# Kernel optimization log

Measured on AMD Instinct MI355X. Metric: run time of the kernel, lower is better.

Reference implementation:

```python
import jax, jax.numpy as jnp
import numpy as np

NEG_SLOPE = 0.2

def gat_conv(x, src, dst, W, a_src, a_dst, bias, num_nodes, heads, out_ch, concat):
    # x: [N, Fin]; W: [Fin, heads*out_ch]; a_src/a_dst: [heads, out_ch]
    h = (x @ W).reshape(num_nodes, heads, out_ch)            # [N,H,C]
    alpha_s = jnp.einsum('nhc,hc->nh', h, a_src)             # [N,H]
    alpha_d = jnp.einsum('nhc,hc->nh', h, a_dst)             # [N,H]
    e = alpha_s[src] + alpha_d[dst]                          # [E,H]
    e = jnp.where(e > 0, e, NEG_SLOPE * e)                   # LeakyReLU
    # segment softmax over incoming edges per destination node
    m = jax.ops.segment_max(e, dst, num_segments=num_nodes)  # [N,H]
    m = jnp.where(jnp.isfinite(m), m, 0.0)
    ee = jnp.exp(e - m[dst])                                 # [E,H]
    s = jax.ops.segment_sum(ee, dst, num_segments=num_nodes) # [N,H]
    alpha = ee / (s[dst] + 1e-16)                            # [E,H]
    out = jax.ops.segment_sum(h[src] * alpha[:, :, None], dst,
                              num_segments=num_nodes)        # [N,H,C]
    if concat:
        out = out.reshape(num_nodes, heads * out_ch)
    else:
        out = out.mean(axis=1)
    return out + bias


def setup_inputs() -> dict:
    key = jax.random.key(0)
    ks = jax.random.split(key, 10)
    N, E = 50000, 800000
    EMB, HID, HEADS, REPR = 128, 128, 8, 64
    C1 = HID // HEADS  # 16
    x = jax.random.normal(ks[0], (N, EMB), dtype=jnp.float32)
    edge_index = jax.random.randint(ks[1], (2, E), 0, N, dtype=jnp.int32)
    sc = 1.0 / np.sqrt(EMB)
    W1 = jax.random.normal(ks[2], (EMB, HEADS * C1), dtype=jnp.float32) * sc
    a1_src = jax.random.normal(ks[3], (HEADS, C1), dtype=jnp.float32) * 0.1
    a1_dst = jax.random.normal(ks[4], (HEADS, C1), dtype=jnp.float32) * 0.1
    b1 = jnp.zeros((HID,), dtype=jnp.float32)
    sc2 = 1.0 / np.sqrt(HID)
    W2 = jax.random.normal(ks[5], (HID, REPR), dtype=jnp.float32) * sc2
    a2_src = jax.random.normal(ks[6], (1, REPR), dtype=jnp.float32) * 0.1
    a2_dst = jax.random.normal(ks[7], (1, REPR), dtype=jnp.float32) * 0.1
    b2 = jnp.zeros((REPR,), dtype=jnp.float32)
    return {"x": x, "edge_index": edge_index,
            "W1": W1, "a1_src": a1_src, "a1_dst": a1_dst, "b1": b1,
            "W2": W2, "a2_src": a2_src, "a2_dst": a2_dst, "b2": b2}


def reference(x, edge_index, W1, a1_src, a1_dst, b1, W2, a2_src, a2_dst, b2):
    N = x.shape[0]
    # PyG GATConv adds self-loops by default
    loops = jnp.arange(N, dtype=edge_index.dtype)
    src = jnp.concatenate([edge_index[0], loops])
    dst = jnp.concatenate([edge_index[1], loops])
    # eval mode: F.dropout(p=0.6) is identity
    h = gat_conv(x, src, dst, W1, a1_src, a1_dst, b1, N,
                 heads=8, out_ch=16, concat=True)
    h = jax.nn.elu(h)
    out = gat_conv(h, src, dst, W2, a2_src, a2_dst, b2, N,
                   heads=1, out_ch=64, concat=True)
    return out
```

## Files before the change

kernel.cpp:

```cpp
#include <hip/hip_runtime.h>
#include <hip/hip_fp16.h>
#include <math.h>


typedef _Float16 f16x8 __attribute__((ext_vector_type(8)));
typedef float f32x4 __attribute__((ext_vector_type(4)));

#define NCHUNK 8
#define MAXBDIV 8192
#define CAP 16384

__device__ __forceinline__ float leaky_exp(float e) {
    e = (e > 0.f) ? e : 0.2f * e;
    return __expf(e);
}

__device__ __forceinline__ void acc16(float w, float4 hv0, float4 hv1,
                                      float* __restrict__ acc) {
    const __half2* p0 = (const __half2*)&hv0;
    const __half2* p1 = (const __half2*)&hv1;
#pragma unroll
    for (int k = 0; k < 4; k++) {
        float2 f = __half22float2(p0[k]);
        acc[2 * k] += w * f.x;
        acc[2 * k + 1] += w * f.y;
    }
#pragma unroll
    for (int k = 0; k < 4; k++) {
        float2 f = __half22float2(p1[k]);
        acc[8 + 2 * k] += w * f.x;
        acc[8 + 2 * k + 1] += w * f.y;
    }
}

__device__ __forceinline__ void acc8(float w, float4 hv,
                                     float* __restrict__ acc) {
    const __half2* hp = (const __half2*)&hv;
#pragma unroll
    for (int k = 0; k < 4; k++) {
        float2 f = __half22float2(hp[k]);
        acc[2 * k] += w * f.x;
        acc[2 * k + 1] += w * f.y;
    }
}

__global__ __launch_bounds__(256) void augw_kernel(const float* __restrict__ W1,
                                                   const float* __restrict__ a1s,
                                                   const float* __restrict__ a1d,
                                                   const float* __restrict__ W2,
                                                   const float* __restrict__ a2s,
                                                   const float* __restrict__ a2d,
                                                   _Float16* __restrict__ W1t,
                                                   _Float16* __restrict__ W2t) {
    int t = threadIdx.x;
    if (blockIdx.x == 0) {
        for (int i = t; i < 144 * 128; i += 256) {
            int c = i >> 7, k = i & 127;
            float v;
            if (c < 128) {
                v = W1[k * 128 + c];
            } else if (c < 136) {
                int h = c - 128; v = 0.f;
#pragma unroll
                for (int j = 0; j < 16; j++) v += W1[k * 128 + h * 16 + j] * a1s[h * 16 + j];
            } else {
                int h = c - 136; v = 0.f;
#pragma unroll
                for (int j = 0; j < 16; j++) v += W1[k * 128 + h * 16 + j] * a1d[h * 16 + j];
            }
            W1t[c * 128 + k] = (_Float16)v;
        }
    } else {
        for (int i = t; i < 80 * 128; i += 256) {
            int c = i >> 7, k = i & 127;
            float v = 0.f;
            if (c < 64) {
                v = W2[k * 64 + c];
            } else if (c == 64) {
                for (int j = 0; j < 64; j++) v += W2[k * 64 + j] * a2s[j];
            } else if (c == 65) {
                for (int j = 0; j < 64; j++) v += W2[k * 64 + j] * a2d[j];
            }
            W2t[c * 128 + k] = (_Float16)v;
        }
    }
}

__global__ __launch_bounds__(256) void gemm1_bucket_kernel(
        const float* __restrict__ x, const _Float16* __restrict__ W1t,
        __half* __restrict__ h1, float* __restrict__ als,
        float* __restrict__ ald, int N, int gridG1,
        const int* __restrict__ src, const int* __restrict__ dst, int E,
        int* __restrict__ bucketCnt, unsigned* __restrict__ pairs) {
    __shared__ _Float16 Xs[64 * 136];
    int t = threadIdx.x;
    if ((int)blockIdx.x >= gridG1) {
        int* lcnt = (int*)Xs;
        int* lbase = lcnt + 64;
        if (t < 64) lcnt[t] = 0;
        __syncthreads();
        int bid = blockIdx.x - gridG1;
        int bdiv = (N + 7) >> 3;
        int i0 = (bid * 256 + t) * 4;
        int s_[4], d_[4], bk[4], rk[4];
        int nv = 0;
        if (i0 + 3 < E) {
            int4 d4 = *(const int4*)(dst + i0);
            int4 s4 = *(const int4*)(src + i0);
            s_[0] = s4.x; s_[1] = s4.y; s_[2] = s4.z; s_[3] = s4.w;
            d_[0] = d4.x; d_[1] = d4.y; d_[2] = d4.z; d_[3] = d4.w;
            nv = 4;
        } else {
            for (int k = i0; k < E && nv < 4; k++) {
                s_[nv] = src[k]; d_[nv] = dst[k]; nv++;
            }
        }
#pragma unroll 4
        for (int u = 0; u < 4; u++) {
            if (u < nv) {
                int b = (s_[u] / bdiv) * 8 + (d_[u] / bdiv);
                bk[u] = b;
                rk[u] = atomicAdd(&lcnt[b], 1);
            }
        }
        __syncthreads();
        if (t < 64) lbase[t] = atomicAdd(&bucketCnt[t * 16], lcnt[t]);
        __syncthreads();
#pragma unroll 4
        for (int k = 0; k < nv; k++) {
            unsigned dlocal = (unsigned)(d_[k] % bdiv);
            pairs[(size_t)bk[k] * CAP + lbase[bk[k]] + rk[k]] =
                (dlocal << 16) | (unsigned)s_[k];
        }
        return;
    }
    int row0 = blockIdx.x * 64;
    for (int i = t; i < 2048; i += 256) {
        int r = i >> 5, c4 = i & 31;
        int gr = row0 + r;
        float4 v = make_float4(0.f, 0.f, 0.f, 0.f);
        if (gr < N) v = *(const float4*)(x + (size_t)gr * 128 + c4 * 4);
        _Float16* dp = Xs + r * 136 + c4 * 4;
        dp[0] = (_Float16)v.x; dp[1] = (_Float16)v.y;
        dp[2] = (_Float16)v.z; dp[3] = (_Float16)v.w;
    }
    __syncthreads();
    int w = t >> 6, L = t & 63, m = L & 15, quad = L >> 4;
    f32x4 acc[9];
#pragma unroll
    for (int f = 0; f < 9; f++) acc[f] = (f32x4){0.f, 0.f, 0.f, 0.f};
    const _Float16* Arow = Xs + (w * 16 + m) * 136 + quad * 8;
    const _Float16* Brow = W1t + m * 128 + quad * 8;
#pragma unroll
    for (int kt = 0; kt < 4; kt++) {
        f16x8 a = *(const f16x8*)(Arow + kt * 32);
#pragma unroll
        for (int f = 0; f < 9; f++) {
            f16x8 b = *(const f16x8*)(Brow + f * 2048 + kt * 32);
            acc[f] = __builtin_amdgcn_mfma_f32_16x16x32_f16(a, b, acc[f], 0, 0, 0);
        }
    }
    int nbase = row0 + w * 16 + quad * 4;
#pragma unroll
    for (int r = 0; r < 4; r++) {
        int n = nbase + r;
        if (n < N) {
            __half* hrow = h1 + (size_t)n * 128 + m;
#pragma unroll
            for (int f = 0; f < 8; f++) hrow[f * 16] = __float2half(acc[f][r]);
            float v = acc[8][r];
            if (m < 8) als[n * 8 + m] = v;
            else ald[n * 8 + (m - 8)] = v;
        }
    }
}

__global__ __launch_bounds__(256) void subhist_kernel(
        const int* __restrict__ bucketCnt, const unsigned* __restrict__ pairs,
        int N, int* __restrict__ subcnt) {
    __shared__ int hist[MAXBDIV];
    int t = threadIdx.x;
    int b = blockIdx.x & 63;
    int j = blockIdx.x >> 6;
    int bdiv = (N + 7) >> 3;
    for (int i = t; i < bdiv; i += 256) hist[i] = 0;
    __syncthreads();
    int cnt = bucketCnt[b * 16];
    int chunk = (cnt + NCHUNK - 1) / NCHUNK;
    int lo = j * chunk;
    int hi = min(lo + chunk, cnt);
    const unsigned* plist = pairs + (size_t)b * CAP;
    for (int i = lo + t; i < hi; i += 256) {
        atomicAdd(&hist[plist[i] >> 16], 1);
    }
    __syncthreads();
    int* out = subcnt + (size_t)(b * NCHUNK + j) * bdiv;
    for (int i = t; i < bdiv; i += 256) out[i] = hist[i];
}

__global__ __launch_bounds__(256) void scan1_kernel(const int* __restrict__ subcnt,
                                                    int N,
                                                    int* __restrict__ rowstart,
                                                    int* __restrict__ blocksum) {
    __shared__ int tmp[256];
    int t = threadIdx.x;
    int i = blockIdx.x * 256 + t;
    int bdiv = (N + 7) >> 3;
    int v = 0;
    if (i < N) {
        int dd = i / bdiv;
        int local = i - dd * bdiv;
#pragma unroll
        for (int so = 0; so < 8; so++) {
            const int* sc = subcnt + ((size_t)(so * 8 + dd) * NCHUNK) * bdiv + local;
#pragma unroll
            for (int j = 0; j < NCHUNK; j++) v += sc[(size_t)j * bdiv];
        }
    }
    tmp[t] = v;
    __syncthreads();
    for (int off = 1; off < 256; off <<= 1) {
        int x = (t >= off) ? tmp[t - off] : 0;
        __syncthreads();
        tmp[t] += x;
        __syncthreads();
    }
    if (i < N) rowstart[i] = tmp[t] - v;
    if (t == 255) blocksum[blockIdx.x] = tmp[t];
}

__global__ __launch_bounds__(256) void scan23_kernel(int* __restrict__ rowstart,
                                                     const int* __restrict__ blocksum,
                                                     int nb,
                                                     int* __restrict__ subcnt,
                                                     int N, int E) {
    __shared__ int sdata[256];
    int t = threadIdx.x;
    int bx = blockIdx.x;
    sdata[t] = (t < nb && t < bx) ? blocksum[t] : 0;
    __syncthreads();
#pragma unroll
    for (int off = 128; off > 0; off >>= 1) {
        if (t < off) sdata[t] += sdata[t + off];
        __syncthreads();
    }
    int offset = sdata[0];
    int i = bx * 256 + t;
    int bdiv = (N + 7) >> 3;
    if (i < N) {
        int v = rowstart[i] + offset;
        rowstart[i] = v;
        int dd = i / bdiv;
        int local = i - dd * bdiv;
        int c = v;
#pragma unroll
        for (int so = 0; so < 8; so++) {
            int* sc = subcnt + ((size_t)(so * 8 + dd) * NCHUNK) * bdiv + local;
#pragma unroll
            for (int j = 0; j < NCHUNK; j++) {
                int cj = sc[(size_t)j * bdiv];
                sc[(size_t)j * bdiv] = c;
                c += cj;
            }
        }
    } else if (i == N) {
        rowstart[N] = E;
    }
}

__global__ __launch_bounds__(256) void scatter_kernel(
        const int* __restrict__ bucketCnt, const unsigned* __restrict__ pairs,
        int N, const int* __restrict__ subcnt, int* __restrict__ esrc) {
    __shared__ int lcur[MAXBDIV];
    int t = threadIdx.x;
    int b = blockIdx.x & 63;
    int j = blockIdx.x >> 6;
    int bdiv = (N + 7) >> 3;
    const int* base = subcnt + (size_t)(b * NCHUNK + j) * bdiv;
    for (int i = t; i < bdiv; i += 256) lcur[i] = base[i];
    __syncthreads();
    int cnt = bucketCnt[b * 16];
    int chunk = (cnt + NCHUNK - 1) / NCHUNK;
    int lo = j * chunk;
    int hi = min(lo + chunk, cnt);
    const unsigned* plist = pairs + (size_t)b * CAP;
    for (int i = lo + t; i < hi; i += 256) {
        unsigned p = plist[i];
        int pos = atomicAdd(&lcur[p >> 16], 1);
        esrc[pos] = (int)(p & 0xFFFFu);
    }
}

__global__ __launch_bounds__(256) void agg1_gemm2_kernel(
        const __half* __restrict__ h1, const float* __restrict__ als,
        const float* __restrict__ ald, const int* __restrict__ rowstart,
        const int* __restrict__ esrc, const float* __restrict__ b1,
        const _Float16* __restrict__ W2t, __half* __restrict__ h2,
        float* __restrict__ al2s, float* __restrict__ al2d, int N) {
    __shared__ _Float16 actS[32 * 136];
    int t = threadIdx.x;
    int lane = t & 63;
    int grp = lane >> 3;
    int q = lane & 7;
    int bdiv = (N + 7) >> 3;
    int lrow = (t >> 6) * 8 + grp;
    int ln = (blockIdx.x >> 3) * 32 + lrow;
    int n = (blockIdx.x & 7) * bdiv + ln;
    bool valid = (ln < bdiv) && (n < N);
    const float4* h1v = (const float4*)h1;
    float acc[16];
#pragma unroll
    for (int k = 0; k < 16; k++) acc[k] = 0.f;
    float wsum = 0.f;
    int beg = 0, end = 0;
    float adv = 0.f;
    if (valid) {
        adv = ald[n * 8 + q];
        float wself = leaky_exp(als[n * 8 + q] + adv);
        wsum = wself;
        acc16(wself, h1v[(size_t)n * 16 + 2 * q], h1v[(size_t)n * 16 + 2 * q + 1], acc);
        beg = rowstart[n];
        end = rowstart[n + 1];
    }
    int j = beg;
    for (; j + 4 <= end; j += 4) {
        int s0 = esrc[j], s1 = esrc[j + 1], s2 = esrc[j + 2], s3 = esrc[j + 3];
        float4 a0 = h1v[(size_t)s0 * 16 + 2 * q], b0 = h1v[(size_t)s0 * 16 + 2 * q + 1];
        float4 a1 = h1v[(size_t)s1 * 16 + 2 * q], b1v = h1v[(size_t)s1 * 16 + 2 * q + 1];
        float4 a2 = h1v[(size_t)s2 * 16 + 2 * q], b2 = h1v[(size_t)s2 * 16 + 2 * q + 1];
        float4 a3 = h1v[(size_t)s3 * 16 + 2 * q], b3 = h1v[(size_t)s3 * 16 + 2 * q + 1];
        float e0 = als[s0 * 8 + q], e1 = als[s1 * 8 + q];
        float e2 = als[s2 * 8 + q], e3 = als[s3 * 8 + q];
        float w0 = leaky_exp(e0 + adv), w1 = leaky_exp(e1 + adv);
        float w2 = leaky_exp(e2 + adv), w3 = leaky_exp(e3 + adv);
        wsum += (w0 + w1) + (w2 + w3);
        acc16(w0, a0, b0, acc);
        acc16(w1, a1, b1v, acc);
        acc16(w2, a2, b2, acc);
        acc16(w3, a3, b3, acc);
    }
    for (; j < end; j++) {
        int s = esrc[j];
        float w = leaky_exp(als[s * 8 + q] + adv);
        wsum += w;
        acc16(w, h1v[(size_t)s * 16 + 2 * q], h1v[(size_t)s * 16 + 2 * q + 1], acc);
    }
    __align__(16) __half2 po[8];
    if (valid) {
        float inv = 1.f / (wsum + 1e-16f);
        const float* bf = b1 + q * 16;
#pragma unroll
        for (int k = 0; k < 8; k++) {
            float o0 = acc[2 * k] * inv + bf[2 * k];
            float o1 = acc[2 * k + 1] * inv + bf[2 * k + 1];
            o0 = (o0 > 0.f) ? o0 : (__expf(o0) - 1.f);
            o1 = (o1 > 0.f) ? o1 : (__expf(o1) - 1.f);
            po[k] = __floats2half2_rn(o0, o1);
        }
    } else {
#pragma unroll
        for (int k = 0; k < 8; k++) po[k] = __floats2half2_rn(0.f, 0.f);
    }
    *(float4*)(actS + lrow * 136 + q * 16) = ((float4*)po)[0];
    *(float4*)(actS + lrow * 136 + q * 16 + 8) = ((float4*)po)[1];
    __syncthreads();
    int w4 = t >> 6;
    int m = lane & 15, quad = lane >> 4;
    int rt = w4 & 1;
    int ctbase = (w4 < 2) ? 0 : 1;
    f32x4 acc2[3];
#pragma unroll
    for (int f = 0; f < 3; f++) acc2[f] = (f32x4){0.f, 0.f, 0.f, 0.f};
    const _Float16* Arow2 = actS + (rt * 16 + m) * 136 + quad * 8;
    const _Float16* Brow2 = W2t + m * 128 + quad * 8;
#pragma unroll
    for (int kt = 0; kt < 4; kt++) {
        f16x8 a = *(const f16x8*)(Arow2 + kt * 32);
#pragma unroll
        for (int f = 0; f < 3; f++) {
            int ctf = ctbase + 2 * f;
            if (ctf < 5) {
                f16x8 bb = *(const f16x8*)(Brow2 + ctf * 2048 + kt * 32);
                acc2[f] = __builtin_amdgcn_mfma_f32_16x16x32_f16(a, bb, acc2[f], 0, 0, 0);
            }
        }
    }
    int secbase = (blockIdx.x & 7) * bdiv;
    int lnbase = (blockIdx.x >> 3) * 32 + rt * 16 + quad * 4;
#pragma unroll
    for (int r = 0; r < 4; r++) {
        int ln2 = lnbase + r;
        int n2 = secbase + ln2;
        if (ln2 < bdiv && n2 < N) {
#pragma unroll
            for (int f = 0; f < 3; f++) {
                int ctf = ctbase + 2 * f;
                if (ctf < 4) {
                    h2[(size_t)n2 * 64 + ctf * 16 + m] = __float2half(acc2[f][r]);
                } else if (ctf == 4) {
                    if (m == 0) al2s[n2] = acc2[f][r];
                    else if (m == 1) al2d[n2] = acc2[f][r];
                }
            }
        }
    }
}

__global__ __launch_bounds__(256) void agg2_kernel(const __half* __restrict__ h2,
                                                   const float* __restrict__ al2s,
                                                   const float* __restrict__ al2d,
                                                   const int* __restrict__ rowstart,
                                                   const int* __restrict__ esrc,
                                                   const float* __restrict__ b2,
                                                   float* __restrict__ out, int N) {
    int t = threadIdx.x;
    int lane = t & 63;
    int grp = lane >> 3;
    int q = lane & 7;
    int bdiv = (N + 7) >> 3;
    int ln = (blockIdx.x >> 3) * 32 + (t >> 6) * 8 + grp;
    if (ln >= bdiv) return;
    int n = (blockIdx.x & 7) * bdiv + ln;
    if (n >= N) return;
    const float4* h2v = (const float4*)h2;
    float adv = al2d[n];
    float acc[8];
#pragma unroll
    for (int k = 0; k < 8; k++) acc[k] = 0.f;
    float wsum = 0.f;
    {
        float w = leaky_exp(al2s[n] + adv);
        wsum += w;
        acc8(w, h2v[(size_t)n * 8 + q], acc);
    }
    int beg = rowstart[n], end = rowstart[n + 1];
    int j = beg;
    for (; j + 4 <= end; j += 4) {
        int s0 = esrc[j], s1 = esrc[j + 1], s2 = esrc[j + 2], s3 = esrc[j + 3];
        float4 a0 = h2v[(size_t)s0 * 8 + q];
        float4 a1 = h2v[(size_t)s1 * 8 + q];
        float4 a2 = h2v[(size_t)s2 * 8 + q];
        float4 a3 = h2v[(size_t)s3 * 8 + q];
        float e0 = al2s[s0], e1 = al2s[s1], e2 = al2s[s2], e3 = al2s[s3];
        float w0 = leaky_exp(e0 + adv), w1 = leaky_exp(e1 + adv);
        float w2 = leaky_exp(e2 + adv), w3 = leaky_exp(e3 + adv);
        wsum += (w0 + w1) + (w2 + w3);
        acc8(w0, a0, acc);
        acc8(w1, a1, acc);
        acc8(w2, a2, acc);
        acc8(w3, a3, acc);
    }
    for (; j < end; j++) {
        int s = esrc[j];
        float w = leaky_exp(al2s[s] + adv);
        wsum += w;
        acc8(w, h2v[(size_t)s * 8 + q], acc);
    }
    float inv = 1.f / (wsum + 1e-16f);
    const float* bf = b2 + q * 8;
    float4* ov = (float4*)(out + (size_t)n * 64 + q * 8);
    ov[0] = make_float4(acc[0] * inv + bf[0], acc[1] * inv + bf[1],
                        acc[2] * inv + bf[2], acc[3] * inv + bf[3]);
    ov[1] = make_float4(acc[4] * inv + bf[4], acc[5] * inv + bf[5],
                        acc[6] * inv + bf[6], acc[7] * inv + bf[7]);
}

extern "C" void kernel_launch(void* const* d_in, const int* in_sizes, int n_in,
                              void* d_out, int out_size, void* d_ws, size_t ws_size,
                              hipStream_t stream) {
    (void)n_in; (void)out_size; (void)ws_size;
    const float* x   = (const float*)d_in[0];
    const int*   ei  = (const int*)d_in[1];
    const float* W1  = (const float*)d_in[2];
    const float* a1s = (const float*)d_in[3];
    const float* a1d = (const float*)d_in[4];
    const float* b1  = (const float*)d_in[5];
    const float* W2  = (const float*)d_in[6];
    const float* a2s = (const float*)d_in[7];
    const float* a2d = (const float*)d_in[8];
    const float* b2  = (const float*)d_in[9];
    float* out = (float*)d_out;

    const int N = in_sizes[0] / 128;
    const int E = in_sizes[1] / 2;
    const int* src = ei;
    const int* dst = ei + E;
    const int bdiv = (N + 7) / 8;

    char* wp = (char*)d_ws;
    auto alloc = [&](size_t bytes) -> void* {
        void* p = (void*)wp;
        wp += (bytes + 255) & ~(size_t)255;
        return p;
    };
    __half* h1   = (__half*)alloc((size_t)N * 128 * 2);
    __half* h2   = (__half*)alloc((size_t)N * 64 * 2 + 64 * 256);
    float* al1s = (float*)alloc((size_t)N * 8 * 4);
    float* al1d = (float*)alloc((size_t)N * 8 * 4);
    float* al2s = (float*)alloc((size_t)N * 4);
    float* al2d = (float*)alloc((size_t)N * 4);
    int* bucketCnt = (int*)alloc(64 * 16 * 4);
    int* subcnt   = (int*)alloc((size_t)64 * NCHUNK * bdiv * 4);
    int* rowstart = (int*)alloc((size_t)(N + 1) * 4);
    int* esrc     = (int*)alloc((size_t)E * 4);
    unsigned* pairs = (unsigned*)alloc((size_t)64 * CAP * 4);
    int* blocksum = (int*)alloc(256 * 4);
    _Float16* W1t = (_Float16*)alloc(144 * 128 * 2);
    _Float16* W2t = (_Float16*)alloc(80 * 128 * 2);

    const int nbScan = (N + 255) / 256;
    const int gridH  = (E + 1023) / 1024;
    const int gridG1 = (N + 63) / 64;
    const int gridAggN = 8 * ((bdiv + 31) / 32);
    const int gridSort = 64 * NCHUNK;

    hipMemsetAsync(bucketCnt, 0, 64 * 16 * 4, stream);

    augw_kernel<<<2, 256, 0, stream>>>(W1, a1s, a1d, W2, a2s, a2d, W1t, W2t);
    gemm1_bucket_kernel<<<gridG1 + gridH, 256, 0, stream>>>(
        x, W1t, h1, al1s, al1d, N, gridG1, src, dst, E, bucketCnt, pairs);
    subhist_kernel<<<gridSort, 256, 0, stream>>>(bucketCnt, pairs, N, subcnt);
    scan1_kernel<<<nbScan, 256, 0, stream>>>(subcnt, N, rowstart, blocksum);
    scan23_kernel<<<(N + 256) / 256, 256, 0, stream>>>(rowstart, blocksum, nbScan,
                                                       subcnt, N, E);
    scatter_kernel<<<gridSort, 256, 0, stream>>>(bucketCnt, pairs, N, subcnt, esrc);

    agg1_gemm2_kernel<<<gridAggN, 256, 0, stream>>>(h1, al1s, al1d, rowstart, esrc,
                                                    b1, W2t, h2, al2s, al2d, N);
    agg2_kernel<<<gridAggN, 256, 0, stream>>>(h2, al2s, al2d, rowstart, esrc, b2, out, N);
}
```

Baseline: 222.7 us.

## Fuse CSR sort/scan/scatter kernels into one cooperative kernel with grid syncs

Replaces four separate launches (subhistogram, two scan passes, scatter) with a single cooperative kernel that uses grid.sync between phases, and halves NCHUNK so the grid is 256 blocks. This removes three kernel launch gaps and shortens the per-node subcount scan loops. The trade-offs are fewer blocks per phase, which means less parallelism in the atomic histogram and scatter, plus the cost of the grid-wide barriers. The cooperative launch also needs all 256 blocks to be co-resident despite the 32KB of LDS each block uses.

After: 339.3 us. 1.52x slower.

```diff
diff --git a/kernel.cpp b/kernel.cpp
--- a/kernel.cpp
+++ b/kernel.cpp
@@ -1,12 +1,15 @@
 #include <hip/hip_runtime.h>
 #include <hip/hip_fp16.h>
+#include <hip/hip_cooperative_groups.h>
 #include <math.h>
+
+namespace cg = cooperative_groups;
 
 
 typedef _Float16 f16x8 __attribute__((ext_vector_type(8)));
 typedef float f32x4 __attribute__((ext_vector_type(4)));
 
-#define NCHUNK 8
+#define NCHUNK 4
 #define MAXBDIV 8192
 #define CAP 16384
 
@@ -175,119 +178,103 @@
     }
 }
 
-__global__ __launch_bounds__(256) void subhist_kernel(
+__global__ __launch_bounds__(256) void sort_kernel(
         const int* __restrict__ bucketCnt, const unsigned* __restrict__ pairs,
-        int N, int* __restrict__ subcnt) {
-    __shared__ int hist[MAXBDIV];
+        int N, int E, int* __restrict__ subcnt, int* __restrict__ rowstart,
+        int* __restrict__ blocksum, int* __restrict__ esrc) {
+    cg::grid_group grid = cg::this_grid();
+    __shared__ int lds[MAXBDIV];
     int t = threadIdx.x;
+    int bdiv = (N + 7) >> 3;
     int b = blockIdx.x & 63;
     int j = blockIdx.x >> 6;
-    int bdiv = (N + 7) >> 3;
-    for (int i = t; i < bdiv; i += 256) hist[i] = 0;
-    __syncthreads();
     int cnt = bucketCnt[b * 16];
     int chunk = (cnt + NCHUNK - 1) / NCHUNK;
     int lo = j * chunk;
     int hi = min(lo + chunk, cnt);
     const unsigned* plist = pairs + (size_t)b * CAP;
+
+    for (int i = t; i < bdiv; i += 256) lds[i] = 0;
+    __syncthreads();
     for (int i = lo + t; i < hi; i += 256) {
-        atomicAdd(&hist[plist[i] >> 16], 1);
+        atomicAdd(&lds[plist[i] >> 16], 1);
     }
     __syncthreads();
-    int* out = subcnt + (size_t)(b * NCHUNK + j) * bdiv;
-    for (int i = t; i < bdiv; i += 256) out[i] = hist[i];
-}
-
-__global__ __launch_bounds__(256) void scan1_kernel(const int* __restrict__ subcnt,
-                                                    int N,
-                                                    int* __restrict__ rowstart,
-                                                    int* __restrict__ blocksum) {
-    __shared__ int tmp[256];
-    int t = threadIdx.x;
-    int i = blockIdx.x * 256 + t;
-    int bdiv = (N + 7) >> 3;
-    int v = 0;
-    if (i < N) {
-        int dd = i / bdiv;
-        int local = i - dd * bdiv;
-#pragma unroll
-        for (int so = 0; so < 8; so++) {
-            const int* sc = subcnt + ((size_t)(so * 8 + dd) * NCHUNK) * bdiv + local;
-#pragma unroll
-            for (int j = 0; j < NCHUNK; j++) v += sc[(size_t)j * bdiv];
-        }
-    }
-    tmp[t] = v;
-    __syncthreads();
-    for (int off = 1; off < 256; off <<= 1) {
-        int x = (t >= off) ? tmp[t - off] : 0;
+    {
+        int* out = subcnt + (size_t)(b * NCHUNK + j) * bdiv;
+        for (int i = t; i < bdiv; i += 256) out[i] = lds[i];
+    }
+    grid.sync();
+
+    int nbScan = (N + 255) / 256;
+    if ((int)blockIdx.x < nbScan) {
+        int i = blockIdx.x * 256 + t;
+        int v = 0;
+        if (i < N) {
+            int dd = i / bdiv;
+            int local = i - dd * bdiv;
+#pragma unroll
+            for (int so = 0; so < 8; so++) {
+                const int* sc = subcnt + ((size_t)(so * 8 + dd) * NCHUNK) * bdiv + local;
+#pragma unroll
+                for (int jj = 0; jj < NCHUNK; jj++) v += sc[(size_t)jj * bdiv];
+            }
+        }
+        lds[t] = v;
         __syncthreads();
-        tmp[t] += x;
+        for (int off = 1; off < 256; off <<= 1) {
+            int xv = (t >= off) ? lds[t - off] : 0;
+            __syncthreads();
+            lds[t] += xv;
+            __syncthreads();
+        }
+        if (i < N) rowstart[i] = lds[t] - v;
+        if (t == 255) blocksum[blockIdx.x] = lds[t];
+    }
+    grid.sync();
+
+    int nb23 = (N + 256) / 256;
+    if ((int)blockIdx.x < nb23) {
+        lds[t] = (t < nbScan && t < (int)blockIdx.x) ? blocksum[t] : 0;
         __syncthreads();
-    }
-    if (i < N) rowstart[i] = tmp[t] - v;
-    if (t == 255) blocksum[blockIdx.x] = tmp[t];
-}
-
-__global__ __launch_bounds__(256) void scan23_kernel(int* __restrict__ rowstart,
-                                                     const int* __restrict__ blocksum,
-                                                     int nb,
-                                                     int* __restrict__ subcnt,
-                                                     int N, int E) {
-    __shared__ int sdata[256];
-    int t = threadIdx.x;
-    int bx = blockIdx.x;
-    sdata[t] = (t < nb && t < bx) ? blocksum[t] : 0;
-    __syncthreads();
-#pragma unroll
-    for (int off = 128; off > 0; off >>= 1) {
-        if (t < off) sdata[t] += sdata[t + off];
+#pragma unroll
+        for (int off = 128; off > 0; off >>= 1) {
+            if (t < off) lds[t] += lds[t + off];
+            __syncthreads();
+        }
+        int offset = lds[0];
+        int i = blockIdx.x * 256 + t;
+        if (i < N) {
+            int v = rowstart[i] + offset;
+            rowstart[i] = v;
+            int dd = i / bdiv;
+            int local = i - dd * bdiv;
+            int c = v;
+#pragma unroll
+            for (int so = 0; so < 8; so++) {
+                int* sc = subcnt + ((size_t)(so * 8 + dd) * NCHUNK) * bdiv + local;
+#pragma unroll
+                for (int jj = 0; jj < NCHUNK; jj++) {
+                    int cj = sc[(size_t)jj * bdiv];
+                    sc[(size_t)jj * bdiv] = c;
+                    c += cj;
+                }
+            }
+        } else if (i == N) {
+            rowstart[N] = E;
+        }
+    }
+    grid.sync();
+
+    {
+        const int* base = subcnt + (size_t)(b * NCHUNK + j) * bdiv;
+        for (int i = t; i < bdiv; i += 256) lds[i] = base[i];
         __syncthreads();
-    }
-    int offset = sdata[0];
-    int i = bx * 256 + t;
-    int bdiv = (N + 7) >> 3;
-    if (i < N) {
-        int v = rowstart[i] + offset;
-        rowstart[i] = v;
-        int dd = i / bdiv;
-        int local = i - dd * bdiv;
-        int c = v;
-#pragma unroll
-        for (int so = 0; so < 8; so++) {
-            int* sc = subcnt + ((size_t)(so * 8 + dd) * NCHUNK) * bdiv + local;
-#pragma unroll
-            for (int j = 0; j < NCHUNK; j++) {
-                int cj = sc[(size_t)j * bdiv];
-                sc[(size_t)j * bdiv] = c;
-                c += cj;
-            }
-        }
-    } else if (i == N) {
-        rowstart[N] = E;
-    }
-}
-
-__global__ __launch_bounds__(256) void scatter_kernel(
-        const int* __restrict__ bucketCnt, const unsigned* __restrict__ pairs,
-        int N, const int* __restrict__ subcnt, int* __restrict__ esrc) {
-    __shared__ int lcur[MAXBDIV];
-    int t = threadIdx.x;
-    int b = blockIdx.x & 63;
-    int j = blockIdx.x >> 6;
-    int bdiv = (N + 7) >> 3;
-    const int* base = subcnt + (size_t)(b * NCHUNK + j) * bdiv;
-    for (int i = t; i < bdiv; i += 256) lcur[i] = base[i];
-    __syncthreads();
-    int cnt = bucketCnt[b * 16];
-    int chunk = (cnt + NCHUNK - 1) / NCHUNK;
-    int lo = j * chunk;
-    int hi = min(lo + chunk, cnt);
-    const unsigned* plist = pairs + (size_t)b * CAP;
-    for (int i = lo + t; i < hi; i += 256) {
-        unsigned p = plist[i];
-        int pos = atomicAdd(&lcur[p >> 16], 1);
-        esrc[pos] = (int)(p & 0xFFFFu);
+        for (int i = lo + t; i < hi; i += 256) {
+            unsigned p = plist[i];
+            int pos = atomicAdd(&lds[p >> 16], 1);
+            esrc[pos] = (int)(p & 0xFFFFu);
+        }
     }
 }
 
@@ -364,10 +351,10 @@
     *(float4*)(actS + lrow * 136 + q * 16) = ((float4*)po)[0];
     *(float4*)(actS + lrow * 136 + q * 16 + 8) = ((float4*)po)[1];
     __syncthreads();
-    int w4 = t >> 6;
+    int w4w = t >> 6;
     int m = lane & 15, quad = lane >> 4;
-    int rt = w4 & 1;
-    int ctbase = (w4 < 2) ? 0 : 1;
+    int rt = w4w & 1;
+    int ctbase = (w4w < 2) ? 0 : 1;
     f32x4 acc2[3];
 #pragma unroll
     for (int f = 0; f < 3; f++) acc2[f] = (f32x4){0.f, 0.f, 0.f, 0.f};
@@ -508,23 +495,23 @@
     _Float16* W1t = (_Float16*)alloc(144 * 128 * 2);
     _Float16* W2t = (_Float16*)alloc(80 * 128 * 2);
 
-    const int nbScan = (N + 255) / 256;
     const int gridH  = (E + 1023) / 1024;
     const int gridG1 = (N + 63) / 64;
     const int gridAggN = 8 * ((bdiv + 31) / 32);
-    const int gridSort = 64 * NCHUNK;
 
     hipMemsetAsync(bucketCnt, 0, 64 * 16 * 4, stream);
 
     augw_kernel<<<2, 256, 0, stream>>>(W1, a1s, a1d, W2, a2s, a2d, W1t, W2t);
     gemm1_bucket_kernel<<<gridG1 + gridH, 256, 0, stream>>>(
         x, W1t, h1, al1s, al1d, N, gridG1, src, dst, E, bucketCnt, pairs);
-    subhist_kernel<<<gridSort, 256, 0, stream>>>(bucketCnt, pairs, N, subcnt);
-    scan1_kernel<<<nbScan, 256, 0, stream>>>(subcnt, N, rowstart, blocksum);
-    scan23_kernel<<<(N + 256) / 256, 256, 0, stream>>>(rowstart, blocksum, nbScan,
-                                                       subcnt, N, E);
-    scatter_kernel<<<gridSort, 256, 0, stream>>>(bucketCnt, pairs, N, subcnt, esrc);
-
+    {
+        int Nv = N, Ev = E;
+        void* args[] = {(void*)&bucketCnt, (void*)&pairs, (void*)&Nv, (void*)&Ev,
+                        (void*)&subcnt, (void*)&rowstart, (void*)&blocksum,
+                        (void*)&esrc};
+        hipLaunchCooperativeKernel((void*)sort_kernel, dim3(64 * NCHUNK),
+                                   dim3(256), args, 0, stream);
+    }
     agg1_gemm2_kernel<<<gridAggN, 256, 0, stream>>>(h1, al1s, al1d, rowstart, esrc,
                                                     b1, W2t, h2, al2s, al2d, N);
     agg2_kernel<<<gridAggN, 256, 0, stream>>>(h2, al2s, al2d, rowstart, esrc, b2, out, N);
```
